# Kernel optimization log

Measured on AMD Instinct MI355X. Metric: run time of the kernel, lower is better.

The kernel has to match this reference:

```python
import jax, jax.numpy as jnp
import numpy as np

SCALE = 0.25
POOL = (7, 7)
SR = 2          # sampling_ratio
EPS = 1e-5      # LayerNorm eps
B, N, C, H, W = 4, 256, 256, 128, 128
D = 1024
IN_DIM = C * POOL[0] * POOL[1]


def _layer_norm(x, g, b):
    m = x.mean(-1, keepdims=True)
    v = ((x - m) ** 2).mean(-1, keepdims=True)
    return (x - m) / jnp.sqrt(v + EPS) * g + b


def _roi_align_one(feat, ys, xs):
    # feat [C,H,W]; ys [N,PH]; xs [N,PW] sample coords in feature-map space
    Cc, Hh, Ww = feat.shape
    y = ys[:, :, None]                      # [N,PH,1]
    x = xs[:, None, :]                      # [N,1,PW]
    valid = (y > -1.0) & (y < Hh) & (x > -1.0) & (x < Ww)  # torchvision semantics
    yc = jnp.clip(y, 0.0, Hh - 1)
    xc = jnp.clip(x, 0.0, Ww - 1)
    y0 = jnp.floor(yc).astype(jnp.int32)
    x0 = jnp.floor(xc).astype(jnp.int32)
    y1 = jnp.minimum(y0 + 1, Hh - 1)
    x1 = jnp.minimum(x0 + 1, Ww - 1)
    ly = yc - y0; lx = xc - x0
    hy = 1.0 - ly; hx = 1.0 - lx
    flat = feat.reshape(Cc, Hh * Ww)
    g = lambda yi, xi: flat[:, yi * Ww + xi]            # [C,N,PH,PW]
    val = (hy * hx) * g(y0, x0) + (hy * lx) * g(y0, x1) \
        + (ly * hx) * g(y1, x0) + (ly * lx) * g(y1, x1)
    return jnp.where(valid, val, 0.0)                    # [C,N,PH,PW]


def roi_align(feats, boxes):
    # feats [B,C,H,W]; boxes [B,N,4] in image coords -> pooled [B,N,C,ph,pw]
    Bb, Cc, Hh, Ww = feats.shape
    ph, pw = POOL
    b = boxes * SCALE
    bx1, by1, bx2, by2 = b[..., 0], b[..., 1], b[..., 2], b[..., 3]
    rw = jnp.maximum(bx2 - bx1, 1.0)
    rh = jnp.maximum(by2 - by1, 1.0)
    bh = rh / ph
    bw = rw / pw
    # sample offset k -> bin k//SR, sub-sample k%SR: (k+0.5)/SR bin-units
    oy = (jnp.arange(ph * SR, dtype=feats.dtype) + 0.5) / SR
    ox = (jnp.arange(pw * SR, dtype=feats.dtype) + 0.5) / SR
    ys = by1[..., None] + bh[..., None] * oy             # [B,N,ph*SR]
    xs = bx1[..., None] + bw[..., None] * ox             # [B,N,pw*SR]
    vals = jax.vmap(_roi_align_one)(feats, ys, xs)       # [B,C,N,PH,PW]
    Nn = boxes.shape[1]
    vals = vals.transpose(0, 2, 1, 3, 4).reshape(Bb, Nn, Cc, ph, SR, pw, SR)
    return vals.mean(axis=(4, 6))                        # avg over 2x2 samples


def setup_inputs() -> dict:
    key = jax.random.key(0)
    ks = jax.random.split(key, 8)
    feats = jax.random.normal(ks[0], (B, C, H, W), dtype=jnp.float32)
    r = jax.random.uniform(ks[1], (B, N, 4), dtype=jnp.float32)
    x1 = r[..., 0] * (512 - 64)
    y1 = r[..., 1] * (512 - 64)
    x2 = x1 + 4.0 + r[..., 2] * 60.0
    y2 = y1 + 4.0 + r[..., 3] * 60.0
    lines_box = jnp.stack([x1, y1, x2, y2], axis=-1)
    img_sizes = jnp.full((B, 2), 512, dtype=jnp.int32)
    W1 = jax.random.normal(ks[2], (IN_DIM, D), dtype=jnp.float32) / np.sqrt(IN_DIM)
    b1 = jnp.zeros((D,), jnp.float32)
    W2 = jax.random.normal(ks[3], (D, D), dtype=jnp.float32) / np.sqrt(D)
    b2 = jnp.zeros((D,), jnp.float32)
    bbox_W = jax.random.normal(ks[4], (4, D), dtype=jnp.float32) / 2.0
    bbox_b = jnp.zeros((D,), jnp.float32)
    ln_bbox_g = jnp.ones((D,), jnp.float32); ln_bbox_b = jnp.zeros((D,), jnp.float32)
    ln_add_g = jnp.ones((D,), jnp.float32); ln_add_b = jnp.zeros((D,), jnp.float32)
    return {"feats": feats, "lines_box": lines_box, "img_sizes": img_sizes,
            "W1": W1, "b1": b1, "W2": W2, "b2": b2,
            "bbox_W": bbox_W, "bbox_b": bbox_b,
            "ln_bbox_g": ln_bbox_g, "ln_bbox_b": ln_bbox_b,
            "ln_add_g": ln_add_g, "ln_add_b": ln_add_b}


def reference(feats, lines_box, img_sizes, W1, b1, W2, b2, bbox_W, bbox_b,
              ln_bbox_g, ln_bbox_b, ln_add_g, ln_add_b):
    Bb = feats.shape[0]
    Hh, Ww = feats.shape[-2:]
    Nn = lines_box.shape[1]
    pooled = roi_align(feats, lines_box).reshape(Bb, Nn, -1)   # [B,N,C*ph*pw]
    h = jax.nn.relu(pooled @ W1 + b1) @ W2 + b2                # [B,N,D]
    # per-image box normalization: x*scale/feats_W, y*scale/feats_H
    norm = SCALE * jnp.array([1.0 / Ww, 1.0 / Hh, 1.0 / Ww, 1.0 / Hh], feats.dtype)
    nb = lines_box * norm
    p = _layer_norm(nb @ bbox_W + bbox_b, ln_bbox_g, ln_bbox_b)
    return _layer_norm(h + p, ln_add_g, ln_add_b)              # [B,N,D]
```

## Files before the change

### kernel.cpp

```cpp
#include <hip/hip_runtime.h>
#include <hip/hip_bf16.h>

typedef __attribute__((ext_vector_type(8))) short short8;
typedef __attribute__((ext_vector_type(4))) float floatx4;

#define AS1(p) ((const __attribute__((address_space(1))) void*)(p))
#define AS3(p) ((__attribute__((address_space(3))) void*)(p))

__device__ __forceinline__ float bf_lo(unsigned u) { return __uint_as_float(u << 16); }
__device__ __forceinline__ float bf_hi(unsigned u) { return __uint_as_float(u & 0xffff0000u); }

__global__ __launch_bounds__(256) void transpose_cast_kernel(
    const float* __restrict__ src, __hip_bfloat16* __restrict__ dst, int R, int C)
{
    __shared__ float tile[32][33];
    const int c0 = blockIdx.x * 32;
    const int r0 = blockIdx.y * 32;
    const int tx = threadIdx.x;
    const int ty = threadIdx.y;
    #pragma unroll
    for (int i = 0; i < 4; ++i)
        tile[ty + i * 8][tx] = src[(size_t)(r0 + ty + i * 8) * C + c0 + tx];
    __syncthreads();
    #pragma unroll
    for (int i = 0; i < 4; ++i) {
        const int c = c0 + ty + i * 8;
        dst[(size_t)c * R + r0 + tx] = __float2bfloat16(tile[tx][ty + i * 8]);
    }
}

__global__ __launch_bounds__(256) void feats_nhwc_kernel(
    const float* __restrict__ src, __hip_bfloat16* __restrict__ dst)
{
    __shared__ float tile[32][33];
    const int hw0 = blockIdx.x * 32;
    const int c0  = blockIdx.y * 32;
    const int b   = blockIdx.z;
    const int tx = threadIdx.x, ty = threadIdx.y;
    #pragma unroll
    for (int i = 0; i < 4; ++i)
        tile[ty + i * 8][tx] = src[((size_t)(b * 256 + c0 + ty + i * 8)) * 16384 + hw0 + tx];
    __syncthreads();
    #pragma unroll
    for (int i = 0; i < 4; ++i)
        dst[((size_t)b * 16384 + hw0 + ty + i * 8) * 256 + c0 + tx] =
            __float2bfloat16(tile[tx][ty + i * 8]);
}

__global__ __launch_bounds__(256) void w1_permute_kernel(
    const float* __restrict__ W1, __hip_bfloat16* __restrict__ W1T)
{
    __shared__ float tile[32][33];
    const int bin = blockIdx.x;
    const int c0  = blockIdx.y * 32;
    const int n0  = blockIdx.z * 32;
    const int tx = threadIdx.x, ty = threadIdx.y;
    #pragma unroll
    for (int i = 0; i < 4; ++i)
        tile[ty + i * 8][tx] = W1[((size_t)(c0 + ty + i * 8) * 49 + bin) * 1024 + n0 + tx];
    __syncthreads();
    #pragma unroll
    for (int i = 0; i < 4; ++i)
        W1T[(size_t)(n0 + ty + i * 8) * 12544 + bin * 256 + c0 + tx] =
            __float2bfloat16(tile[tx][ty + i * 8]);
}

__global__ __launch_bounds__(256) void roi_kernel4(
    const __hip_bfloat16* __restrict__ featsT, const float* __restrict__ boxes,
    __hip_bfloat16* __restrict__ pooled)
{
    __shared__ int   sy0[14], sy1[14], sx0[14], sx1[14];
    __shared__ float sly[14], svy[14], slx[14], svx[14];
    const int tid  = threadIdx.x;
    const int bn   = blockIdx.x >> 1;
    const int half = blockIdx.x & 1;
    if (tid < 28) {
        const int  i   = tid % 14;
        const bool isx = tid >= 14;
        const float lo = boxes[bn * 4 + (isx ? 0 : 1)] * 0.25f;
        const float hi = boxes[bn * 4 + (isx ? 2 : 3)] * 0.25f;
        const float szb = fmaxf(hi - lo, 1.0f) * (1.0f / 7.0f);
        const float coord = lo + szb * ((i + 0.5f) * 0.5f);
        const float valid = (coord > -1.0f && coord < 128.0f) ? 1.0f : 0.0f;
        const float cc = fminf(fmaxf(coord, 0.0f), 127.0f);
        const int i0 = (int)floorf(cc);
        const int i1 = min(i0 + 1, 127);
        const float l = cc - (float)i0;
        if (isx) { sx0[i] = i0; sx1[i] = i1; slx[i] = l; svx[i] = valid; }
        else     { sy0[i] = i0; sy1[i] = i1; sly[i] = l; svy[i] = valid; }
    }
    __syncthreads();
    const int wave = tid >> 6;
    const int lane = tid & 63;
    const int sub  = lane >> 5;
    const int co   = lane & 31;
    const int b    = bn >> 8;
    const __hip_bfloat16* fb = featsT + (size_t)b * 4194304 + co * 8;
    __hip_bfloat16* po = pooled + (size_t)bn * 12544 + co * 8;

    const int pstart = (half ? 12 : 0) + wave;
    const int pend   = half ? 25 : 12;
    for (int p = pstart; p < pend; p += 4) {
        int bin = 2 * p + sub;
        if (bin > 48) bin = 48;
        const int ph = (bin * 37) >> 8;
        const int pw = bin - ph * 7;
        float s0 = 0.f, s1 = 0.f, s2 = 0.f, s3 = 0.f;
        float s4 = 0.f, s5 = 0.f, s6 = 0.f, s7 = 0.f;
        #pragma unroll
        for (int sy = 0; sy < 2; ++sy) {
            const int iy = ph * 2 + sy;
            const int y0 = sy0[iy], y1 = sy1[iy];
            const float ly = sly[iy], wy = svy[iy];
            const float hy = 1.f - ly;
            #pragma unroll
            for (int sx = 0; sx < 2; ++sx) {
                const int ix = pw * 2 + sx;
                const int x0 = sx0[ix], x1 = sx1[ix];
                const float lx = slx[ix], wx = svx[ix];
                const float hx = 1.f - lx;
                const uint4 u00 = *(const uint4*)(fb + (((y0 << 7) + x0) * 256));
                const uint4 u01 = *(const uint4*)(fb + (((y0 << 7) + x1) * 256));
                const uint4 u10 = *(const uint4*)(fb + (((y1 << 7) + x0) * 256));
                const uint4 u11 = *(const uint4*)(fb + (((y1 << 7) + x1) * 256));
                const float wv  = wy * wx;
                const float w00 = hy * hx * wv, w01 = hy * lx * wv;
                const float w10 = ly * hx * wv, w11 = ly * lx * wv;
                s0 += w00 * bf_lo(u00.x) + w01 * bf_lo(u01.x) + w10 * bf_lo(u10.x) + w11 * bf_lo(u11.x);
                s1 += w00 * bf_hi(u00.x) + w01 * bf_hi(u01.x) + w10 * bf_hi(u10.x) + w11 * bf_hi(u11.x);
                s2 += w00 * bf_lo(u00.y) + w01 * bf_lo(u01.y) + w10 * bf_lo(u10.y) + w11 * bf_lo(u11.y);
                s3 += w00 * bf_hi(u00.y) + w01 * bf_hi(u01.y) + w10 * bf_hi(u10.y) + w11 * bf_hi(u11.y);
                s4 += w00 * bf_lo(u00.z) + w01 * bf_lo(u01.z) + w10 * bf_lo(u10.z) + w11 * bf_lo(u11.z);
                s5 += w00 * bf_hi(u00.z) + w01 * bf_hi(u01.z) + w10 * bf_hi(u10.z) + w11 * bf_hi(u11.z);
                s6 += w00 * bf_lo(u00.w) + w01 * bf_lo(u01.w) + w10 * bf_lo(u10.w) + w11 * bf_lo(u11.w);
                s7 += w00 * bf_hi(u00.w) + w01 * bf_hi(u01.w) + w10 * bf_hi(u10.w) + w11 * bf_hi(u11.w);
            }
        }
        union { __hip_bfloat16 h[8]; uint4 u; } o;
        o.h[0] = __float2bfloat16(s0 * 0.25f);
        o.h[1] = __float2bfloat16(s1 * 0.25f);
        o.h[2] = __float2bfloat16(s2 * 0.25f);
        o.h[3] = __float2bfloat16(s3 * 0.25f);
        o.h[4] = __float2bfloat16(s4 * 0.25f);
        o.h[5] = __float2bfloat16(s5 * 0.25f);
        o.h[6] = __float2bfloat16(s6 * 0.25f);
        o.h[7] = __float2bfloat16(s7 * 0.25f);
        *(uint4*)(po + bin * 256) = o.u;
    }
}

__global__ __launch_bounds__(512, 2) void gemm1_8phase(
    const __hip_bfloat16* __restrict__ A,
    const __hip_bfloat16* __restrict__ BT,
    __hip_bfloat16* __restrict__ Cpart)
{
    constexpr int K = 12544;
    constexpr int KCHUNK = 896;
    constexpr int NKT = KCHUNK / 64;
    constexpr int ITERS = NKT / 2;

    __shared__ char lds[131072];

    const int bid = blockIdx.x;
    const int sid = (bid & 7) * 28 + (bid >> 3);
    const int z  = sid >> 4;
    const int bx = sid & 3;
    const int by = (sid >> 2) & 3;
    const int m0 = by << 8;
    const int n0 = bx << 8;
    const int k0 = z * KCHUNK;

    const int tid  = threadIdx.x;
    const int lane = tid & 63;
    const int wave = tid >> 6;
    const int wm   = wave >> 2;
    const int wn   = wave & 3;
    const int l15  = lane & 15;
    const int kq   = (lane >> 4) << 3;

    floatx4 acc[8][4] = {};
    short8 bf[4][2];

    auto stage = [&](const __hip_bfloat16* gsrc, int ldsoff) {
        #pragma unroll
        for (int j = 0; j < 2; ++j) {
            const int lin = j * 8192 + tid * 16;
            const int r   = lin >> 7;
            const int cs  = ((lin & 127) ^ (((lin >> 9) & 1) << 5)) >> 1;
            __builtin_amdgcn_global_load_lds(AS1(gsrc + (size_t)r * K + cs),
                                             AS3(lds + ldsoff + lin), 16, 0, 0);
        }
    };

#define PHASE(SLOT, MQ, FIRSTB, STAGE_STMT)                                        \
    {                                                                               \
        if (FIRSTB) {                                                               \
            _Pragma("unroll")                                                       \
            for (int nf = 0; nf < 4; ++nf) {                                        \
                const int nl = wn * 64 + nf * 16 + l15;                             \
                const int bh = nl >> 7, br = nl & 127;                              \
                _Pragma("unroll")                                                   \
                for (int ks = 0; ks < 2; ++ks)                                      \
                    bf[nf][ks] = *(const short8*)(lds + (SLOT) * 65536 + 32768      \
                        + bh * 16384 + br * 128                                     \
                        + (((ks * 32 + kq) * 2) ^ ((br & 4) << 3)));                \
            }                                                                       \
        }                                                                           \
        short8 af[2][2];                                                            \
        _Pragma("unroll")                                                           \
        for (int mf = 0; mf < 2; ++mf) {                                            \
            const int ar = (MQ) * 32 + mf * 16 + l15;                               \
            _Pragma("unroll")                                                       \
            for (int ks = 0; ks < 2; ++ks)                                          \
                af[mf][ks] = *(const short8*)(lds + (SLOT) * 65536 + wm * 16384     \
                    + ar * 128 + (((ks * 32 + kq) * 2) ^ ((ar & 4) << 3)));         \
        }                                                                           \
        STAGE_STMT;                                                                 \
        __builtin_amdgcn_s_barrier();                                               \
        asm volatile("s_waitcnt lgkmcnt(0)" ::: "memory");                          \
        __builtin_amdgcn_s_setprio(1);                                              \
        _Pragma("unroll")                                                           \
        for (int mf = 0; mf < 2; ++mf)                                              \
            _Pragma("unroll")                                                       \
            for (int nf = 0; nf < 4; ++nf)                                          \
                _Pragma("unroll")                                                   \
                for (int ks = 0; ks < 2; ++ks)                                      \
                    acc[(MQ) * 2 + mf][nf] = __builtin_amdgcn_mfma_f32_16x16x32_bf16( \
                        af[mf][ks], bf[nf][ks], acc[(MQ) * 2 + mf][nf], 0, 0, 0);   \
        __builtin_amdgcn_s_setprio(0);                                              \
        __builtin_amdgcn_s_barrier();                                               \
    }

    stage(BT + (size_t)n0 * K + k0,               32768);
    stage(BT + (size_t)(n0 + 128) * K + k0,       32768 + 16384);
    stage(A  + (size_t)m0 * K + k0,               0);
    stage(A  + (size_t)(m0 + 128) * K + k0,       16384);
    stage(BT + (size_t)n0 * K + k0 + 64,          65536 + 32768);
    stage(BT + (size_t)(n0 + 128) * K + k0 + 64,  65536 + 32768 + 16384);
    asm volatile("s_waitcnt vmcnt(4)" ::: "memory");
    __builtin_amdgcn_s_barrier();

    for (int it = 0; it < ITERS; ++it) {
        const int t1 = 2 * it + 1;
        int t2 = 2 * it + 2; if (t2 > NKT - 1) t2 = NKT - 1;
        int t3 = 2 * it + 3; if (t3 > NKT - 1) t3 = NKT - 1;
        PHASE(0, 0, true,  stage(A  + (size_t)m0 * K + k0 + t1 * 64,          65536));
        PHASE(0, 1, false, stage(A  + (size_t)(m0 + 128) * K + k0 + t1 * 64,  65536 + 16384));
        PHASE(0, 2, false, stage(BT + (size_t)n0 * K + k0 + t2 * 64,          32768));
        PHASE(0, 3, false, stage(BT + (size_t)(n0 + 128) * K + k0 + t2 * 64,  32768 + 16384));
        asm volatile("s_waitcnt vmcnt(4)" ::: "memory");
        PHASE(1, 0, true,  stage(A  + (size_t)m0 * K + k0 + t2 * 64,          0));
        PHASE(1, 1, false, stage(A  + (size_t)(m0 + 128) * K + k0 + t2 * 64,  16384));
        PHASE(1, 2, false, stage(BT + (size_t)n0 * K + k0 + t3 * 64,          65536 + 32768));
        PHASE(1, 3, false, stage(BT + (size_t)(n0 + 128) * K + k0 + t3 * 64,  65536 + 32768 + 16384));
        asm volatile("s_waitcnt vmcnt(4)" ::: "memory");
    }
#undef PHASE

    __hip_bfloat16* cp = Cpart + (size_t)z * (1024 * 1024) + (size_t)m0 * 1024 + n0;
    const int r4 = (lane >> 4) << 2;
    #pragma unroll
    for (int mi = 0; mi < 8; ++mi)
        #pragma unroll
        for (int nf = 0; nf < 4; ++nf)
            #pragma unroll
            for (int r = 0; r < 4; ++r)
                cp[(size_t)(wm * 128 + mi * 16 + r4 + r) * 1024 + wn * 64 + nf * 16 + l15] =
                    __float2bfloat16(acc[mi][nf][r]);
}

__global__ __launch_bounds__(256) void gemm_bf16_kernel(
    const __hip_bfloat16* __restrict__ A,
    const __hip_bfloat16* __restrict__ BT,
    __hip_bfloat16* __restrict__ Cpart,
    int Mdim, int Ndim, int K, int kChunk)
{
    __shared__ __hip_bfloat16 lsA[128 * 64];
    __shared__ __hip_bfloat16 lsB[128 * 64];
    const int tid  = threadIdx.x;
    const int lane = tid & 63;
    const int wave = tid >> 6;
    const int wrow = (wave >> 1) << 6;
    const int wcol = (wave & 1) << 6;
    const int m0 = blockIdx.y << 7;
    const int n0 = blockIdx.x << 7;
    const int k0 = blockIdx.z * kChunk;

    floatx4 acc[4][4] = {};

    const int strow = tid >> 3;
    const int stk   = (tid & 7) << 3;
    const __hip_bfloat16* aSrc = A  + (size_t)(m0 + strow) * K + k0 + stk;
    const __hip_bfloat16* bSrc = BT + (size_t)(n0 + strow) * K + k0 + stk;
    __hip_bfloat16* ldsA = lsA + tid * 8;
    __hip_bfloat16* ldsB = lsB + tid * 8;
    const size_t rowJump = (size_t)32 * K;

    const int row16 = lane & 15;
    const int kg    = (lane >> 4) << 3;
    const int nk = kChunk >> 6;
    for (int kk = 0; kk < nk; ++kk) {
        __syncthreads();
        #pragma unroll
        for (int g = 0; g < 4; ++g) {
            __builtin_amdgcn_global_load_lds(AS1(aSrc + g * rowJump), AS3(ldsA + g * 2048), 16, 0, 0);
            __builtin_amdgcn_global_load_lds(AS1(bSrc + g * rowJump), AS3(ldsB + g * 2048), 16, 0, 0);
        }
        __syncthreads();
        #pragma unroll
        for (int ks = 0; ks < 2; ++ks) {
            short8 af[4], bfr[4];
            #pragma unroll
            for (int m = 0; m < 4; ++m)
                af[m] = *(const short8*)(lsA + (wrow + m * 16 + row16) * 64 + ks * 32 + kg);
            #pragma unroll
            for (int n = 0; n < 4; ++n)
                bfr[n] = *(const short8*)(lsB + (wcol + n * 16 + row16) * 64 + ks * 32 + kg);
            #pragma unroll
            for (int m = 0; m < 4; ++m)
                #pragma unroll
                for (int n = 0; n < 4; ++n)
                    acc[m][n] = __builtin_amdgcn_mfma_f32_16x16x32_bf16(af[m], bfr[n], acc[m][n], 0, 0, 0);
        }
        aSrc += 64; bSrc += 64;
    }
    __hip_bfloat16* cp = Cpart + (size_t)blockIdx.z * Mdim * Ndim + (size_t)m0 * Ndim + n0;
    const int r4 = (lane >> 4) << 2;
    #pragma unroll
    for (int m = 0; m < 4; ++m)
        #pragma unroll
        for (int n = 0; n < 4; ++n)
            #pragma unroll
            for (int r = 0; r < 4; ++r)
                cp[(size_t)(wrow + m * 16 + r4 + r) * Ndim + (wcol + n * 16 + row16)] =
                    __float2bfloat16(acc[m][n][r]);
}

__global__ __launch_bounds__(256) void reduce_relu_kernel(
    const __hip_bfloat16* __restrict__ part, const float* __restrict__ bias,
    __hip_bfloat16* __restrict__ out, int nsplit)
{
    const size_t MN = 1024 * 1024;
    const int idx = (blockIdx.x * 256 + threadIdx.x) * 8;
    float s[8] = {};
    for (int z = 0; z < nsplit; ++z) {
        const uint4 v = *(const uint4*)(part + z * MN + idx);
        s[0] += bf_lo(v.x); s[1] += bf_hi(v.x);
        s[2] += bf_lo(v.y); s[3] += bf_hi(v.y);
        s[4] += bf_lo(v.z); s[5] += bf_hi(v.z);
        s[6] += bf_lo(v.w); s[7] += bf_hi(v.w);
    }
    const int jb = idx & 1023;
    const floatx4 b0 = *(const floatx4*)(bias + jb);
    const floatx4 b1v = *(const floatx4*)(bias + jb + 4);
    union { __hip_bfloat16 h[8]; uint4 u; } o;
    #pragma unroll
    for (int i = 0; i < 4; ++i) {
        const float v0 = s[i] + b0[i];
        o.h[i] = __float2bfloat16(v0 > 0.0f ? v0 : 0.0f);
    }
    #pragma unroll
    for (int i = 0; i < 4; ++i) {
        const float v1 = s[4 + i] + b1v[i];
        o.h[4 + i] = __float2bfloat16(v1 > 0.0f ? v1 : 0.0f);
    }
    *(uint4*)(out + idx) = o.u;
}

__device__ inline void block_stats(float s, float ss, float* red, float& mean, float& rstd)
{
    #pragma unroll
    for (int o = 32; o > 0; o >>= 1) {
        s  += __shfl_down(s, o, 64);
        ss += __shfl_down(ss, o, 64);
    }
    const int wave = threadIdx.x >> 6;
    const int lane = threadIdx.x & 63;
    __syncthreads();
    if (lane == 0) { red[wave] = s; red[8 + wave] = ss; }
    __syncthreads();
    const float a = red[0] + red[1] + red[2] + red[3];
    const float b = red[8] + red[9] + red[10] + red[11];
    mean = a * (1.0f / 1024.0f);
    const float var = b * (1.0f / 1024.0f) - mean * mean;
    rstd = rsqrtf(var + 1e-5f);
}

__global__ __launch_bounds__(256) void final_kernel(
    const __hip_bfloat16* __restrict__ part2, const float* __restrict__ b2,
    const float* __restrict__ boxes,
    const float* __restrict__ bboxW, const float* __restrict__ bboxb,
    const float* __restrict__ g1, const float* __restrict__ bb1,
    const float* __restrict__ g2, const float* __restrict__ bb2,
    float* __restrict__ out)
{
    __shared__ float red[16];
    const int row = blockIdx.x;
    const int j0 = threadIdx.x * 4;
    const size_t MN = 1024 * 1024;

    floatx4 h = *(const floatx4*)(b2 + j0);
    #pragma unroll
    for (int z = 0; z < 4; ++z) {
        const uint2 v = *(const uint2*)(part2 + z * MN + (size_t)row * 1024 + j0);
        h[0] += bf_lo(v.x); h[1] += bf_hi(v.x);
        h[2] += bf_lo(v.y); h[3] += bf_hi(v.y);
    }

    const float sc = 0.25f / 128.0f;
    const float nb0 = boxes[row * 4 + 0] * sc;
    const float nb1 = boxes[row * 4 + 1] * sc;
    const float nb2 = boxes[row * 4 + 2] * sc;
    const float nb3 = boxes[row * 4 + 3] * sc;

    floatx4 p = *(const floatx4*)(bboxb + j0);
    p += nb0 * *(const floatx4*)(bboxW + j0);
    p += nb1 * *(const floatx4*)(bboxW + 1024 + j0);
    p += nb2 * *(const floatx4*)(bboxW + 2048 + j0);
    p += nb3 * *(const floatx4*)(bboxW + 3072 + j0);

    float mean, rstd;
    block_stats(p[0] + p[1] + p[2] + p[3],
                p[0]*p[0] + p[1]*p[1] + p[2]*p[2] + p[3]*p[3], red, mean, rstd);
    const floatx4 pg = *(const floatx4*)(g1 + j0);
    const floatx4 pb = *(const floatx4*)(bb1 + j0);
    floatx4 x;
    #pragma unroll
    for (int i = 0; i < 4; ++i)
        x[i] = h[i] + ((p[i] - mean) * rstd * pg[i] + pb[i]);

    block_stats(x[0] + x[1] + x[2] + x[3],
                x[0]*x[0] + x[1]*x[1] + x[2]*x[2] + x[3]*x[3], red, mean, rstd);
    const floatx4 og = *(const floatx4*)(g2 + j0);
    const floatx4 ob = *(const floatx4*)(bb2 + j0);
    floatx4 o;
    #pragma unroll
    for (int i = 0; i < 4; ++i)
        o[i] = (x[i] - mean) * rstd * og[i] + ob[i];
    *(floatx4*)(out + (size_t)row * 1024 + j0) = o;
}

extern "C" void kernel_launch(void* const* d_in, const int* in_sizes, int n_in,
                              void* d_out, int out_size, void* d_ws, size_t ws_size,
                              hipStream_t stream)
{
    const float* feats = (const float*)d_in[0];
    const float* boxes = (const float*)d_in[1];
    const float* W1    = (const float*)d_in[3];
    const float* b1    = (const float*)d_in[4];
    const float* W2    = (const float*)d_in[5];
    const float* b2    = (const float*)d_in[6];
    const float* bboxW = (const float*)d_in[7];
    const float* bboxb = (const float*)d_in[8];
    const float* g1    = (const float*)d_in[9];
    const float* bb1   = (const float*)d_in[10];
    const float* g2    = (const float*)d_in[11];
    const float* bb2   = (const float*)d_in[12];
    float* out = (float*)d_out;

    char* ws = (char*)d_ws;
    __hip_bfloat16* W1T    = (__hip_bfloat16*)(ws);
    __hip_bfloat16* W2T    = (__hip_bfloat16*)(ws + 25690112);
    __hip_bfloat16* pooled = (__hip_bfloat16*)(ws + 27787264);
    __hip_bfloat16* part1  = (__hip_bfloat16*)(ws + 53477376);
    __hip_bfloat16* part2  = part1;
    __hip_bfloat16* featsT = (__hip_bfloat16*)(ws + 53477376);
    __hip_bfloat16* A2     = (__hip_bfloat16*)(ws + 87031808);

    feats_nhwc_kernel<<<dim3(512, 8, 4), dim3(32, 8), 0, stream>>>(feats, featsT);
    w1_permute_kernel<<<dim3(49, 8, 32), dim3(32, 8), 0, stream>>>(W1, W1T);
    transpose_cast_kernel<<<dim3(32, 32), dim3(32, 8), 0, stream>>>(W2, W2T, 1024, 1024);
    roi_kernel4<<<2048, 256, 0, stream>>>(featsT, boxes, pooled);
    gemm1_8phase<<<224, 512, 0, stream>>>(pooled, W1T, part1);
    reduce_relu_kernel<<<512, 256, 0, stream>>>(part1, b1, A2, 14);
    gemm_bf16_kernel<<<dim3(8, 8, 4), 256, 0, stream>>>(A2, W2T, part2, 1024, 1024, 1024, 256);
    final_kernel<<<1024, 256, 0, stream>>>(part2, b2, boxes, bboxW, bboxb, g1, bb1, g2, bb2, out);
}
```

Measured before the change: 112.2 us.

## Replace 8-phase GEMM1 with 4-stage K=32 ring-buffered pipeline and XCD-aware split-K mapping

Rewrites the split-K GEMM1 main loop to use K-tiles of 32 in a 4-slot LDS ring with a prefetch distance of 3 tiles, in place of two 64-wide double-buffered slots. Each tile is split into two MFMA half-phases, one per half of the A rows. The block-to-tile mapping is changed so that all 16 output tiles of a K-chunk sit on the same XCD, which should improve L2 reuse of the A and B panels. The launch grows to 256 blocks and the 32 surplus blocks return early. The new layout uses a different swizzle and adds barriers per K step, trading deeper latency hiding for more synchronisation and a finer K granularity.

```diff
diff --git a/kernel.cpp b/kernel.cpp
--- a/kernel.cpp
+++ b/kernel.cpp
@@ -149,25 +149,25 @@
     }
 }
 
-__global__ __launch_bounds__(512, 2) void gemm1_8phase(
+__global__ __launch_bounds__(512, 2) void gemm1_deep(
     const __hip_bfloat16* __restrict__ A,
     const __hip_bfloat16* __restrict__ BT,
     __hip_bfloat16* __restrict__ Cpart)
 {
     constexpr int K = 12544;
     constexpr int KCHUNK = 896;
-    constexpr int NKT = KCHUNK / 64;
-    constexpr int ITERS = NKT / 2;
+    constexpr int NKT = 28;
 
     __shared__ char lds[131072];
 
-    const int bid = blockIdx.x;
-    const int sid = (bid & 7) * 28 + (bid >> 3);
-    const int z  = sid >> 4;
-    const int bx = sid & 3;
-    const int by = (sid >> 2) & 3;
-    const int m0 = by << 8;
-    const int n0 = bx << 8;
+    const int bid  = blockIdx.x;
+    const int xcd  = bid & 7;
+    const int sl   = bid >> 3;
+    const int z    = xcd + 8 * (sl >> 4);
+    if (z >= 14) return;
+    const int tile = sl & 15;
+    const int by = tile >> 2, bx = tile & 3;
+    const int m0 = by << 8, n0 = bx << 8;
     const int k0 = z * KCHUNK;
 
     const int tid  = threadIdx.x;
@@ -176,86 +176,75 @@
     const int wm   = wave >> 2;
     const int wn   = wave & 3;
     const int l15  = lane & 15;
-    const int kq   = (lane >> 4) << 3;
+    const int kb   = (lane >> 4) << 4;
 
     floatx4 acc[8][4] = {};
-    short8 bf[4][2];
-
-    auto stage = [&](const __hip_bfloat16* gsrc, int ldsoff) {
+
+    auto stage = [&](const __hip_bfloat16* gbase, int kt, int ldsoff) {
+        const __hip_bfloat16* gsrc = gbase + kt * 32;
         #pragma unroll
         for (int j = 0; j < 2; ++j) {
             const int lin = j * 8192 + tid * 16;
-            const int r   = lin >> 7;
-            const int cs  = ((lin & 127) ^ (((lin >> 9) & 1) << 5)) >> 1;
+            const int r   = lin >> 6;
+            const int cs  = ((lin & 63) ^ ((r & 3) << 4)) >> 1;
             __builtin_amdgcn_global_load_lds(AS1(gsrc + (size_t)r * K + cs),
                                              AS3(lds + ldsoff + lin), 16, 0, 0);
         }
     };
-
-#define PHASE(SLOT, MQ, FIRSTB, STAGE_STMT)                                        \
-    {                                                                               \
-        if (FIRSTB) {                                                               \
-            _Pragma("unroll")                                                       \
-            for (int nf = 0; nf < 4; ++nf) {                                        \
-                const int nl = wn * 64 + nf * 16 + l15;                             \
-                const int bh = nl >> 7, br = nl & 127;                              \
-                _Pragma("unroll")                                                   \
-                for (int ks = 0; ks < 2; ++ks)                                      \
-                    bf[nf][ks] = *(const short8*)(lds + (SLOT) * 65536 + 32768      \
-                        + bh * 16384 + br * 128                                     \
-                        + (((ks * 32 + kq) * 2) ^ ((br & 4) << 3)));                \
-            }                                                                       \
-        }                                                                           \
-        short8 af[2][2];                                                            \
-        _Pragma("unroll")                                                           \
-        for (int mf = 0; mf < 2; ++mf) {                                            \
-            const int ar = (MQ) * 32 + mf * 16 + l15;                               \
-            _Pragma("unroll")                                                       \
-            for (int ks = 0; ks < 2; ++ks)                                          \
-                af[mf][ks] = *(const short8*)(lds + (SLOT) * 65536 + wm * 16384     \
-                    + ar * 128 + (((ks * 32 + kq) * 2) ^ ((ar & 4) << 3)));         \
-        }                                                                           \
-        STAGE_STMT;                                                                 \
-        __builtin_amdgcn_s_barrier();                                               \
-        asm volatile("s_waitcnt lgkmcnt(0)" ::: "memory");                          \
-        __builtin_amdgcn_s_setprio(1);                                              \
-        _Pragma("unroll")                                                           \
-        for (int mf = 0; mf < 2; ++mf)                                              \
-            _Pragma("unroll")                                                       \
-            for (int nf = 0; nf < 4; ++nf)                                          \
-                _Pragma("unroll")                                                   \
-                for (int ks = 0; ks < 2; ++ks)                                      \
-                    acc[(MQ) * 2 + mf][nf] = __builtin_amdgcn_mfma_f32_16x16x32_bf16( \
-                        af[mf][ks], bf[nf][ks], acc[(MQ) * 2 + mf][nf], 0, 0, 0);   \
-        __builtin_amdgcn_s_setprio(0);                                              \
-        __builtin_amdgcn_s_barrier();                                               \
-    }
-
-    stage(BT + (size_t)n0 * K + k0,               32768);
-    stage(BT + (size_t)(n0 + 128) * K + k0,       32768 + 16384);
-    stage(A  + (size_t)m0 * K + k0,               0);
-    stage(A  + (size_t)(m0 + 128) * K + k0,       16384);
-    stage(BT + (size_t)n0 * K + k0 + 64,          65536 + 32768);
-    stage(BT + (size_t)(n0 + 128) * K + k0 + 64,  65536 + 32768 + 16384);
-    asm volatile("s_waitcnt vmcnt(4)" ::: "memory");
+    const __hip_bfloat16* Abase = A  + (size_t)m0 * K + k0;
+    const __hip_bfloat16* Bbase = BT + (size_t)n0 * K + k0;
+
+    for (int t = 0; t < 3; ++t) {
+        stage(Abase, t, t * 32768);
+        stage(Bbase, t, t * 32768 + 16384);
+    }
+    asm volatile("s_waitcnt vmcnt(8)" ::: "memory");
     __builtin_amdgcn_s_barrier();
 
-    for (int it = 0; it < ITERS; ++it) {
-        const int t1 = 2 * it + 1;
-        int t2 = 2 * it + 2; if (t2 > NKT - 1) t2 = NKT - 1;
-        int t3 = 2 * it + 3; if (t3 > NKT - 1) t3 = NKT - 1;
-        PHASE(0, 0, true,  stage(A  + (size_t)m0 * K + k0 + t1 * 64,          65536));
-        PHASE(0, 1, false, stage(A  + (size_t)(m0 + 128) * K + k0 + t1 * 64,  65536 + 16384));
-        PHASE(0, 2, false, stage(BT + (size_t)n0 * K + k0 + t2 * 64,          32768));
-        PHASE(0, 3, false, stage(BT + (size_t)(n0 + 128) * K + k0 + t2 * 64,  32768 + 16384));
-        asm volatile("s_waitcnt vmcnt(4)" ::: "memory");
-        PHASE(1, 0, true,  stage(A  + (size_t)m0 * K + k0 + t2 * 64,          0));
-        PHASE(1, 1, false, stage(A  + (size_t)(m0 + 128) * K + k0 + t2 * 64,  16384));
-        PHASE(1, 2, false, stage(BT + (size_t)n0 * K + k0 + t3 * 64,          65536 + 32768));
-        PHASE(1, 3, false, stage(BT + (size_t)(n0 + 128) * K + k0 + t3 * 64,  65536 + 32768 + 16384));
-        asm volatile("s_waitcnt vmcnt(4)" ::: "memory");
-    }
-#undef PHASE
+    for (int t = 0; t < NKT; ++t) {
+        const int sbase = (t & 3) * 32768;
+        const int pf    = (t + 3 < NKT) ? (t + 3) : (NKT - 1);
+        const int pfdst = ((t + 3) & 3) * 32768;
+        short8 bf[4], af[4];
+        #pragma unroll
+        for (int nf = 0; nf < 4; ++nf) {
+            const int br = wn * 64 + nf * 16 + l15;
+            bf[nf] = *(const short8*)(lds + sbase + 16384 + br * 64 + (kb ^ ((br & 3) << 4)));
+        }
+        #pragma unroll
+        for (int mf = 0; mf < 4; ++mf) {
+            const int ar = wm * 128 + mf * 16 + l15;
+            af[mf] = *(const short8*)(lds + sbase + ar * 64 + (kb ^ ((ar & 3) << 4)));
+        }
+        stage(Abase, pf, pfdst);
+        __builtin_amdgcn_s_barrier();
+        asm volatile("s_waitcnt lgkmcnt(0)" ::: "memory");
+        __builtin_amdgcn_s_setprio(1);
+        #pragma unroll
+        for (int mf = 0; mf < 4; ++mf)
+            #pragma unroll
+            for (int nf = 0; nf < 4; ++nf)
+                acc[mf][nf] = __builtin_amdgcn_mfma_f32_16x16x32_bf16(af[mf], bf[nf], acc[mf][nf], 0, 0, 0);
+        __builtin_amdgcn_s_setprio(0);
+        __builtin_amdgcn_s_barrier();
+        #pragma unroll
+        for (int mf = 0; mf < 4; ++mf) {
+            const int ar = wm * 128 + 64 + mf * 16 + l15;
+            af[mf] = *(const short8*)(lds + sbase + ar * 64 + (kb ^ ((ar & 3) << 4)));
+        }
+        stage(Bbase, pf, pfdst + 16384);
+        asm volatile("s_waitcnt vmcnt(8)" ::: "memory");
+        __builtin_amdgcn_s_barrier();
+        asm volatile("s_waitcnt lgkmcnt(0)" ::: "memory");
+        __builtin_amdgcn_s_setprio(1);
+        #pragma unroll
+        for (int mf = 0; mf < 4; ++mf)
+            #pragma unroll
+            for (int nf = 0; nf < 4; ++nf)
+                acc[4 + mf][nf] = __builtin_amdgcn_mfma_f32_16x16x32_bf16(af[mf], bf[nf], acc[4 + mf][nf], 0, 0, 0);
+        __builtin_amdgcn_s_setprio(0);
+        __builtin_amdgcn_s_barrier();
+    }
 
     __hip_bfloat16* cp = Cpart + (size_t)z * (1024 * 1024) + (size_t)m0 * 1024 + n0;
     const int r4 = (lane >> 4) << 2;
@@ -471,7 +460,7 @@
     w1_permute_kernel<<<dim3(49, 8, 32), dim3(32, 8), 0, stream>>>(W1, W1T);
     transpose_cast_kernel<<<dim3(32, 32), dim3(32, 8), 0, stream>>>(W2, W2T, 1024, 1024);
     roi_kernel4<<<2048, 256, 0, stream>>>(featsT, boxes, pooled);
-    gemm1_8phase<<<224, 512, 0, stream>>>(pooled, W1T, part1);
+    gemm1_deep<<<256, 512, 0, stream>>>(pooled, W1T, part1);
     reduce_relu_kernel<<<512, 256, 0, stream>>>(part1, b1, A2, 14);
     gemm_bf16_kernel<<<dim3(8, 8, 4), 256, 0, stream>>>(A2, W2T, part2, 1024, 1024, 1024, 256);
     final_kernel<<<1024, 256, 0, stream>>>(part2, b2, boxes, bboxW, bboxb, g1, bb1, g2, bb2, out);
```

Measured after the change: 117.0 us. 4.3% more time.

## Swizzle GEMM LDS layouts fully, remap blocks per XCD, move vmcnt waits into phases

Applied to the files above, without the earlier changes.

Both GEMM kernels switch their LDS layouts to a full 8-way XOR swizzle on row bits, applied both when staging and when loading fragments, to cut LDS bank conflicts. gemm1 block IDs are remapped so that every K-split chunk z shares one XCD across all 16 output tiles. The grid grows to 256 with early exit for invalid z. The vmcnt wait moves inside the last phase before its barrier. Risks are the idle padded blocks and a possible change in how the waits line up with the barriers.

```diff
diff --git a/kernel.cpp b/kernel.cpp
--- a/kernel.cpp
+++ b/kernel.cpp
@@ -156,18 +156,19 @@
 {
     constexpr int K = 12544;
     constexpr int KCHUNK = 896;
-    constexpr int NKT = KCHUNK / 64;
-    constexpr int ITERS = NKT / 2;
+    constexpr int NKT = 14;
+    constexpr int ITERS = 7;
 
     __shared__ char lds[131072];
 
     const int bid = blockIdx.x;
-    const int sid = (bid & 7) * 28 + (bid >> 3);
-    const int z  = sid >> 4;
-    const int bx = sid & 3;
-    const int by = (sid >> 2) & 3;
-    const int m0 = by << 8;
-    const int n0 = bx << 8;
+    const int xcd = bid & 7;
+    const int sl  = bid >> 3;
+    const int z   = xcd + 8 * (sl >> 4);
+    if (z >= 14) return;
+    const int tile = sl & 15;
+    const int by = tile >> 2, bx = tile & 3;
+    const int m0 = by << 8, n0 = bx << 8;
     const int k0 = z * KCHUNK;
 
     const int tid  = threadIdx.x;
@@ -186,13 +187,13 @@
         for (int j = 0; j < 2; ++j) {
             const int lin = j * 8192 + tid * 16;
             const int r   = lin >> 7;
-            const int cs  = ((lin & 127) ^ (((lin >> 9) & 1) << 5)) >> 1;
+            const int cs  = ((lin & 127) ^ ((r & 7) << 4)) >> 1;
             __builtin_amdgcn_global_load_lds(AS1(gsrc + (size_t)r * K + cs),
                                              AS3(lds + ldsoff + lin), 16, 0, 0);
         }
     };
 
-#define PHASE(SLOT, MQ, FIRSTB, STAGE_STMT)                                        \
+#define PHASE(SLOT, MQ, FIRSTB, STAGE_STMT, VM)                                    \
     {                                                                               \
         if (FIRSTB) {                                                               \
             _Pragma("unroll")                                                       \
@@ -203,7 +204,7 @@
                 for (int ks = 0; ks < 2; ++ks)                                      \
                     bf[nf][ks] = *(const short8*)(lds + (SLOT) * 65536 + 32768      \
                         + bh * 16384 + br * 128                                     \
-                        + (((ks * 32 + kq) * 2) ^ ((br & 4) << 3)));                \
+                        + (((ks * 32 + kq) * 2) ^ ((br & 7) << 4)));                \
             }                                                                       \
         }                                                                           \
         short8 af[2][2];                                                            \
@@ -213,7 +214,7 @@
             _Pragma("unroll")                                                       \
             for (int ks = 0; ks < 2; ++ks)                                          \
                 af[mf][ks] = *(const short8*)(lds + (SLOT) * 65536 + wm * 16384     \
-                    + ar * 128 + (((ks * 32 + kq) * 2) ^ ((ar & 4) << 3)));         \
+                    + ar * 128 + (((ks * 32 + kq) * 2) ^ ((ar & 7) << 4)));         \
         }                                                                           \
         STAGE_STMT;                                                                 \
         __builtin_amdgcn_s_barrier();                                               \
@@ -228,6 +229,7 @@
                     acc[(MQ) * 2 + mf][nf] = __builtin_amdgcn_mfma_f32_16x16x32_bf16( \
                         af[mf][ks], bf[nf][ks], acc[(MQ) * 2 + mf][nf], 0, 0, 0);   \
         __builtin_amdgcn_s_setprio(0);                                              \
+        if (VM) asm volatile("s_waitcnt vmcnt(4)" ::: "memory");                    \
         __builtin_amdgcn_s_barrier();                                               \
     }
 
@@ -244,16 +246,14 @@
         const int t1 = 2 * it + 1;
         int t2 = 2 * it + 2; if (t2 > NKT - 1) t2 = NKT - 1;
         int t3 = 2 * it + 3; if (t3 > NKT - 1) t3 = NKT - 1;
-        PHASE(0, 0, true,  stage(A  + (size_t)m0 * K + k0 + t1 * 64,          65536));
-        PHASE(0, 1, false, stage(A  + (size_t)(m0 + 128) * K + k0 + t1 * 64,  65536 + 16384));
-        PHASE(0, 2, false, stage(BT + (size_t)n0 * K + k0 + t2 * 64,          32768));
-        PHASE(0, 3, false, stage(BT + (size_t)(n0 + 128) * K + k0 + t2 * 64,  32768 + 16384));
-        asm volatile("s_waitcnt vmcnt(4)" ::: "memory");
-        PHASE(1, 0, true,  stage(A  + (size_t)m0 * K + k0 + t2 * 64,          0));
-        PHASE(1, 1, false, stage(A  + (size_t)(m0 + 128) * K + k0 + t2 * 64,  16384));
-        PHASE(1, 2, false, stage(BT + (size_t)n0 * K + k0 + t3 * 64,          65536 + 32768));
-        PHASE(1, 3, false, stage(BT + (size_t)(n0 + 128) * K + k0 + t3 * 64,  65536 + 32768 + 16384));
-        asm volatile("s_waitcnt vmcnt(4)" ::: "memory");
+        PHASE(0, 0, true,  stage(A  + (size_t)m0 * K + k0 + t1 * 64,          65536),          0);
+        PHASE(0, 1, false, stage(A  + (size_t)(m0 + 128) * K + k0 + t1 * 64,  65536 + 16384),  0);
+        PHASE(0, 2, false, stage(BT + (size_t)n0 * K + k0 + t2 * 64,          32768),          0);
+        PHASE(0, 3, false, stage(BT + (size_t)(n0 + 128) * K + k0 + t2 * 64,  32768 + 16384),  1);
+        PHASE(1, 0, true,  stage(A  + (size_t)m0 * K + k0 + t2 * 64,          0),              0);
+        PHASE(1, 1, false, stage(A  + (size_t)(m0 + 128) * K + k0 + t2 * 64,  16384),          0);
+        PHASE(1, 2, false, stage(BT + (size_t)n0 * K + k0 + t3 * 64,          65536 + 32768),  0);
+        PHASE(1, 3, false, stage(BT + (size_t)(n0 + 128) * K + k0 + t3 * 64,  65536 + 32768 + 16384), 1);
     }
 #undef PHASE
 
@@ -289,9 +289,9 @@
     floatx4 acc[4][4] = {};
 
     const int strow = tid >> 3;
-    const int stk   = (tid & 7) << 3;
-    const __hip_bfloat16* aSrc = A  + (size_t)(m0 + strow) * K + k0 + stk;
-    const __hip_bfloat16* bSrc = BT + (size_t)(n0 + strow) * K + k0 + stk;
+    const int scol  = ((tid & 7) ^ (strow & 7)) << 3;
+    const __hip_bfloat16* aSrc = A  + (size_t)(m0 + strow) * K + k0 + scol;
+    const __hip_bfloat16* bSrc = BT + (size_t)(n0 + strow) * K + k0 + scol;
     __hip_bfloat16* ldsA = lsA + tid * 8;
     __hip_bfloat16* ldsB = lsB + tid * 8;
     const size_t rowJump = (size_t)32 * K;
@@ -311,11 +311,15 @@
         for (int ks = 0; ks < 2; ++ks) {
             short8 af[4], bfr[4];
             #pragma unroll
-            for (int m = 0; m < 4; ++m)
-                af[m] = *(const short8*)(lsA + (wrow + m * 16 + row16) * 64 + ks * 32 + kg);
-            #pragma unroll
-            for (int n = 0; n < 4; ++n)
-                bfr[n] = *(const short8*)(lsB + (wcol + n * 16 + row16) * 64 + ks * 32 + kg);
+            for (int m = 0; m < 4; ++m) {
+                const int ar = wrow + m * 16 + row16;
+                af[m] = *(const short8*)(lsA + ar * 64 + ((ks * 32 + kg) ^ ((ar & 7) << 3)));
+            }
+            #pragma unroll
+            for (int n = 0; n < 4; ++n) {
+                const int br = wcol + n * 16 + row16;
+                bfr[n] = *(const short8*)(lsB + br * 64 + ((ks * 32 + kg) ^ ((br & 7) << 3)));
+            }
             #pragma unroll
             for (int m = 0; m < 4; ++m)
                 #pragma unroll
@@ -471,7 +475,7 @@
     w1_permute_kernel<<<dim3(49, 8, 32), dim3(32, 8), 0, stream>>>(W1, W1T);
     transpose_cast_kernel<<<dim3(32, 32), dim3(32, 8), 0, stream>>>(W2, W2T, 1024, 1024);
     roi_kernel4<<<2048, 256, 0, stream>>>(featsT, boxes, pooled);
-    gemm1_8phase<<<224, 512, 0, stream>>>(pooled, W1T, part1);
+    gemm1_8phase<<<256, 512, 0, stream>>>(pooled, W1T, part1);
     reduce_relu_kernel<<<512, 256, 0, stream>>>(part1, b1, A2, 14);
     gemm_bf16_kernel<<<dim3(8, 8, 4), 256, 0, stream>>>(A2, W2T, part2, 1024, 1024, 1024, 256);
     final_kernel<<<1024, 256, 0, stream>>>(part2, b2, boxes, bboxW, bboxb, g1, bb1, g2, bb2, out);
```

Result: no change. 112.0 us (-0.2%).
